# Optimization experiments

Hardware: AMD Instinct MI355X
Metric: run time of the kernel (lower is better)

The kernel has to match this reference:

```python
import jax, jax.numpy as jnp
import numpy as np

# Marching-cubes corner ordering (standard MC vertex order). The original CUDA
# kernel uses a fixed corner->bit mapping; any fixed permutation only permutes
# the 256 topology columns, the math is identical.
CORNER_OFFSETS = [(0, 0, 0), (1, 0, 0), (1, 1, 0), (0, 1, 0),
                  (0, 0, 1), (1, 0, 1), (1, 1, 1), (0, 1, 1)]
T = 256  # number of marching-cubes topology cases


def setup_inputs() -> dict:
    key = jax.random.key(0)
    # occupancy probabilities on the (W+1,H+1,D+1) grid, W=H=D=64
    occupancy = jax.random.uniform(key, (65, 65, 65), dtype=jnp.float32)
    return {"occupancy": occupancy}


def reference(occupancy):
    Wd, Hd, Dd = (occupancy.shape[0] - 1, occupancy.shape[1] - 1, occupancy.shape[2] - 1)
    # Gather the 8 corner occupancies of every cell: [N, 8], N = W*H*D
    corners = jnp.stack(
        [occupancy[dx:dx + Wd, dy:dy + Hd, dz:dz + Dd].reshape(-1)
         for dx, dy, dz in CORNER_OFFSETS], axis=-1)
    # bits[t, c] = c-th bit of topology case t
    bits = jnp.asarray(((np.arange(T)[:, None] >> np.arange(8)[None, :]) & 1).astype(bool))
    # topology[n, t] = prod_c (p_c if bit set else 1 - p_c)
    topo = jnp.ones((corners.shape[0], T), dtype=occupancy.dtype)
    for c in range(8):  # fixed tiny loop over the 8 corners
        p = corners[:, c:c + 1]                      # [N, 1]
        topo = topo * jnp.where(bits[:, c][None, :], p, 1.0 - p)
    return topo  # [W*H*D, 256]
```

## Files before the change

kernel.cpp:

```cpp
#include <hip/hip_runtime.h>


__global__ __launch_bounds__(256) void
occ_topo_kernel(const float* __restrict__ occ, float* __restrict__ out, int n_cells)
{
    const int lane   = threadIdx.x & 63;
    const int waveInBlk = threadIdx.x >> 6;
    const int wavesPerBlk = blockDim.x >> 6;
    const int totalWaves  = gridDim.x * wavesPerBlk;
    int wave_id = blockIdx.x * wavesPerBlk + waveInBlk;

    const int S1 = 65, S2 = 65 * 65;

    for (int cell = wave_id; cell < n_cells; cell += totalWaves) {
        int z = cell & 63;
        int y = (cell >> 6) & 63;
        int x = cell >> 12;
        int base = x * S2 + y * S1 + z;

        float p0 = occ[base];
        float p1 = occ[base + S2];
        float p2 = occ[base + S2 + S1];
        float p3 = occ[base + S1];
        float p4 = occ[base + 1];
        float p5 = occ[base + S2 + 1];
        float p6 = occ[base + S2 + S1 + 1];
        float p7 = occ[base + S1 + 1];

        float f2 = (lane & 1)  ? p2 : 1.0f - p2;
        float f3 = (lane & 2)  ? p3 : 1.0f - p3;
        float f4 = (lane & 4)  ? p4 : 1.0f - p4;
        float f5 = (lane & 8)  ? p5 : 1.0f - p5;
        float f6 = (lane & 16) ? p6 : 1.0f - p6;
        float f7 = (lane & 32) ? p7 : 1.0f - p7;
        float bp = ((f2 * f3) * (f4 * f5)) * (f6 * f7);

        float q0 = 1.0f - p0;
        float q1 = 1.0f - p1;
        float4 v;
        v.x = bp * (q0 * q1);
        v.y = bp * (p0 * q1);
        v.z = bp * (q0 * p1);
        v.w = bp * (p0 * p1);

        float4* outp = reinterpret_cast<float4*>(out + (size_t)cell * 256) + lane;
        *outp = v;
    }
}

extern "C" void kernel_launch(void* const* d_in, const int* in_sizes, int n_in,
                              void* d_out, int out_size, void* d_ws, size_t ws_size,
                              hipStream_t stream)
{
    const float* occ = (const float*)d_in[0];
    float* out = (float*)d_out;
    const int n_cells = 64 * 64 * 64;

    const int block = 256;
    const int grid  = 2048;
    occ_topo_kernel<<<grid, block, 0, stream>>>(occ, out, n_cells);
}
```

Before: 273.7 us.

## Use scalar corner loads, nontemporal stores, and two-cell unrolled loop

Makes the per-cell base address wave-uniform with readfirstlane so the eight corner loads can become scalar loads. Output stores become nontemporal to bypass cache retention for the large write-only result. The grid-stride loop is unrolled by two so the loads for two cells are issued before either is computed, overlapping load latency. The kernel is dominated by writing the 268 MB output, so the gains available from the load side are likely small.

```diff
diff --git a/kernel.cpp b/kernel.cpp
--- a/kernel.cpp
+++ b/kernel.cpp
@@ -1,50 +1,71 @@
 #include <hip/hip_runtime.h>
 
+
+typedef float vfloat4 __attribute__((ext_vector_type(4)));
+
+struct Corners { float p[8]; };
+
+__device__ __forceinline__ Corners load_cell(const float* __restrict__ occ, int cell)
+{
+    const int S1 = 65, S2 = 65 * 65;
+    int z = cell & 63;
+    int y = (cell >> 6) & 63;
+    int x = cell >> 12;
+    int base = __builtin_amdgcn_readfirstlane(x * S2 + y * S1 + z);
+    const float* c = occ + base;
+    Corners r;
+    r.p[0] = c[0];           r.p[4] = c[1];
+    r.p[3] = c[S1];          r.p[7] = c[S1 + 1];
+    r.p[1] = c[S2];          r.p[5] = c[S2 + 1];
+    r.p[2] = c[S2 + S1];     r.p[6] = c[S2 + S1 + 1];
+    return r;
+}
+
+__device__ __forceinline__ void emit_cell(const Corners& cr, int lane,
+                                          float* __restrict__ out, int cell)
+{
+    float p0 = cr.p[0], p1 = cr.p[1], p2 = cr.p[2], p3 = cr.p[3];
+    float p4 = cr.p[4], p5 = cr.p[5], p6 = cr.p[6], p7 = cr.p[7];
+
+    float f2 = (lane & 1)  ? p2 : 1.0f - p2;
+    float f3 = (lane & 2)  ? p3 : 1.0f - p3;
+    float f4 = (lane & 4)  ? p4 : 1.0f - p4;
+    float f5 = (lane & 8)  ? p5 : 1.0f - p5;
+    float f6 = (lane & 16) ? p6 : 1.0f - p6;
+    float f7 = (lane & 32) ? p7 : 1.0f - p7;
+    float bp = ((f2 * f3) * (f4 * f5)) * (f6 * f7);
+
+    float q0 = 1.0f - p0;
+    float q1 = 1.0f - p1;
+    vfloat4 v;
+    v.x = bp * (q0 * q1);
+    v.y = bp * (p0 * q1);
+    v.z = bp * (q0 * p1);
+    v.w = bp * (p0 * p1);
+
+    vfloat4* outp = reinterpret_cast<vfloat4*>(out + (size_t)cell * 256) + lane;
+    __builtin_nontemporal_store(v, outp);
+}
 
 __global__ __launch_bounds__(256) void
 occ_topo_kernel(const float* __restrict__ occ, float* __restrict__ out, int n_cells)
 {
-    const int lane   = threadIdx.x & 63;
-    const int waveInBlk = threadIdx.x >> 6;
+    const int lane        = threadIdx.x & 63;
+    const int waveInBlk   = threadIdx.x >> 6;
     const int wavesPerBlk = blockDim.x >> 6;
     const int totalWaves  = gridDim.x * wavesPerBlk;
     int wave_id = blockIdx.x * wavesPerBlk + waveInBlk;
 
-    const int S1 = 65, S2 = 65 * 65;
-
-    for (int cell = wave_id; cell < n_cells; cell += totalWaves) {
-        int z = cell & 63;
-        int y = (cell >> 6) & 63;
-        int x = cell >> 12;
-        int base = x * S2 + y * S1 + z;
-
-        float p0 = occ[base];
-        float p1 = occ[base + S2];
-        float p2 = occ[base + S2 + S1];
-        float p3 = occ[base + S1];
-        float p4 = occ[base + 1];
-        float p5 = occ[base + S2 + 1];
-        float p6 = occ[base + S2 + S1 + 1];
-        float p7 = occ[base + S1 + 1];
-
-        float f2 = (lane & 1)  ? p2 : 1.0f - p2;
-        float f3 = (lane & 2)  ? p3 : 1.0f - p3;
-        float f4 = (lane & 4)  ? p4 : 1.0f - p4;
-        float f5 = (lane & 8)  ? p5 : 1.0f - p5;
-        float f6 = (lane & 16) ? p6 : 1.0f - p6;
-        float f7 = (lane & 32) ? p7 : 1.0f - p7;
-        float bp = ((f2 * f3) * (f4 * f5)) * (f6 * f7);
-
-        float q0 = 1.0f - p0;
-        float q1 = 1.0f - p1;
-        float4 v;
-        v.x = bp * (q0 * q1);
-        v.y = bp * (p0 * q1);
-        v.z = bp * (q0 * p1);
-        v.w = bp * (p0 * p1);
-
-        float4* outp = reinterpret_cast<float4*>(out + (size_t)cell * 256) + lane;
-        *outp = v;
+    int cell = wave_id;
+    for (; cell + totalWaves < n_cells; cell += 2 * totalWaves) {
+        Corners a = load_cell(occ, cell);
+        Corners b = load_cell(occ, cell + totalWaves);
+        emit_cell(a, lane, out, cell);
+        emit_cell(b, lane, out, cell + totalWaves);
+    }
+    if (cell < n_cells) {
+        Corners a = load_cell(occ, cell);
+        emit_cell(a, lane, out, cell);
     }
 }
 
```

Measured after the change: 275.5 us. Within noise of the previous version (+0.7%).
